# Optimization experiments

Measured on AMD Instinct MI355X. Metric: run time of the kernel, lower is better.

The kernel has to match this reference:

```python
import jax, jax.numpy as jnp
import numpy as np

N, D_IN, D, E, B = 30000, 512, 512, 300000, 4096
N_RES, N_DNN = 2, 2
EPS = 1e-5


def _ln(x, g, b):
    mu = jnp.mean(x, axis=-1, keepdims=True)
    var = jnp.mean((x - mu) ** 2, axis=-1, keepdims=True)
    return (x - mu) * jax.lax.rsqrt(var + EPS) * g + b


def setup_inputs() -> dict:
    key = jax.random.key(0)
    ks = jax.random.split(key, 16)
    s = 1.0 / np.sqrt(D)
    inp = {
        "node_feat": jax.random.normal(ks[0], (N, D_IN), jnp.float32),
        "edge_hop0": jax.random.randint(ks[1], (2, E), 0, N, jnp.int32),
        "edge_hop1": jax.random.randint(ks[2], (2, E), 0, N, jnp.int32),
        "target_idx": jax.random.randint(ks[3], (B,), 0, N, jnp.int32),
        # node transform
        "Wt": jax.random.normal(ks[4], (D_IN, D), jnp.float32) / np.sqrt(D_IN),
        "bt": jnp.zeros((D,), jnp.float32),
        # GATConv (shared across both hops, one relation)
        "Wf": jax.random.normal(ks[5], (D, D), jnp.float32) * s,
        "bf": jnp.zeros((D,), jnp.float32),
        "w_att": jax.random.normal(ks[6], (2 * D,), jnp.float32) * s,
        "b_att": jnp.zeros((), jnp.float32),
        "gat_bias": jnp.zeros((D,), jnp.float32),
        # Res_DNN
        "Wp": jax.random.normal(ks[7], (D, D), jnp.float32) * s,
        "bp": jnp.zeros((D,), jnp.float32),
        "dnn_W": jax.random.normal(ks[8], (N_RES, N_DNN, D, D), jnp.float32) * s,
        "dnn_b": jnp.zeros((N_RES, N_DNN, D), jnp.float32),
        "dnn_g": jnp.ones((N_RES, N_DNN, D), jnp.float32),
        "dnn_beta": jnp.zeros((N_RES, N_DNN, D), jnp.float32),
        "res_g": jnp.ones((N_RES, D), jnp.float32),
        "res_beta": jnp.zeros((N_RES, D), jnp.float32),
        "Wc": jax.random.normal(ks[9], (D, 1), jnp.float32) * s,
        "bc": jnp.zeros((1,), jnp.float32),
    }
    return inp


def _gat(feat, edges, Wf, bf, w_att, b_att, gat_bias):
    # dst and src are the same node set / same features here
    h = feat @ Wf + bf                      # [N, D]
    di, si = edges[0], edges[1]             # [E], [E]
    # att(concat(dst_h, src_h)) == dst_h @ w[:D] + src_h @ w[D:] + b
    sd = h @ w_att[:D]                      # [N]
    ss = h @ w_att[D:]                      # [N]
    e = jnp.tanh(sd[di] + ss[si] + b_att)   # [E]
    # sparse softmax per destination row
    m = jax.ops.segment_max(e, di, num_segments=N)
    a = jnp.exp(e - m[di])
    denom = jax.ops.segment_sum(a, di, num_segments=N)
    alpha = a / denom[di]                   # [E]
    # sparse-mm aggregation
    out = jax.ops.segment_sum(alpha[:, None] * h[si], di, num_segments=N)
    return out + gat_bias


def reference(node_feat, edge_hop0, edge_hop1, target_idx, Wt, bt, Wf, bf,
              w_att, b_att, gat_bias, Wp, bp, dnn_W, dnn_b, dnn_g, dnn_beta,
              res_g, res_beta, Wc, bc):
    # node-type feature transform (dropout is identity at inference)
    feat = node_feat @ Wt + bt              # [N, D]
    # hops processed from last to first: hop1 then hop0
    for edges in (edge_hop1, edge_hop0):
        g = _gat(feat, edges, Wf, bf, w_att, b_att, gat_bias)
        feat = (feat + g) * 0.5             # mean of stacked [orig, gat_out]
    h = feat[target_idx]                    # [B, D]
    # Res_DNN head
    h = h @ Wp + bp
    for r in range(N_RES):
        sc = h
        for i in range(N_DNN):
            h = _ln(jnp.tanh(h @ dnn_W[r, i] + dnn_b[r, i]), dnn_g[r, i], dnn_beta[r, i])
        h = _ln(jnp.tanh(sc + h), res_g[r], res_beta[r])
    logits = h @ Wc + bc                    # [B, 1]
    return jax.nn.sigmoid(logits)
```

## Files before the change

kernel.cpp:

```cpp
#include <hip/hip_runtime.h>

#define D 512
typedef unsigned short ushort_t;
typedef __attribute__((ext_vector_type(8))) short bf16x8;
typedef __attribute__((ext_vector_type(4))) float f32x4;

static __device__ __forceinline__ ushort_t f2bf(float f) {
  unsigned u = __float_as_uint(f);
  u += 0x7fffu + ((u >> 16) & 1u);
  return (ushort_t)(u >> 16);
}
static __device__ __forceinline__ float bf2f(ushort_t h) {
  return __uint_as_float(((unsigned)h) << 16);
}

static __device__ __forceinline__ void gld_lds16(const void* g, void* lds) {
  __builtin_amdgcn_global_load_lds(
      (const __attribute__((address_space(1))) unsigned int*)g,
      (__attribute__((address_space(3))) unsigned int*)lds, 16, 0, 0);
}

__global__ __launch_bounds__(256) void pack_weight(
    const float* __restrict__ W, ushort_t* __restrict__ out, int K, int N, int nmat) {
  int i = blockIdx.x * 256 + threadIdx.x;
  const int per = K * N;
  if (i >= per * nmat) return;
  const int mat = i / per;
  const int r = i - mat * per;
  const int k = r / N, n = r - k * N;
  const int nt = n >> 4, col = n & 15, kt = k >> 5, kg = (k >> 3) & 3, j = k & 7;
  out[(size_t)mat * per + (((size_t)nt * (K >> 5) + kt) << 9) + ((kg << 4) + col) * 8 + j] =
      f2bf(W[(size_t)mat * per + r]);
}

__global__ __launch_bounds__(256) void conv_bf16_pad(
    const float* __restrict__ in, ushort_t* __restrict__ out, int M, int Mp, int K) {
  const size_t i4 = ((size_t)blockIdx.x * 256 + threadIdx.x) * 4;
  if (i4 >= (size_t)Mp * K) return;
  const int row = (int)(i4 / K);
  ushort4 o;
  if (row < M) {
    const float4 v = *reinterpret_cast<const float4*>(&in[i4]);
    o.x = f2bf(v.x); o.y = f2bf(v.y); o.z = f2bf(v.z); o.w = f2bf(v.w);
  } else {
    o.x = o.y = o.z = o.w = 0;
  }
  *reinterpret_cast<ushort4*>(&out[i4]) = o;
}

__global__ __launch_bounds__(256) void gemm_mfma(
    const ushort_t* __restrict__ A, const ushort_t* __restrict__ Bp,
    const float* __restrict__ bias, ushort_t* __restrict__ C16, int N, int K) {
  __shared__ __align__(16) ushort_t As[2][8 * 512];
  __shared__ __align__(16) ushort_t Bs[2][8 * 512];
  const int nwg = gridDim.x;
  const int q = nwg >> 3, rm = nwg & 7;
  const int xcd = blockIdx.x & 7, kk = blockIdx.x >> 3;
  const int lin = (xcd < rm ? xcd * (q + 1) : rm * (q + 1) + (xcd - rm) * q) + kk;
  const int m0 = (lin >> 2) * 128;
  const int n0 = (lin & 3) * 128;
  const int tid = threadIdx.x;
  const int lane = tid & 63;
  const int wid = tid >> 6;
  const int wm = wid >> 1, wn = wid & 1;
  const int arow = lane & 15;
  const int akoff = (lane >> 4) * 8;
  const int kt32 = K >> 5;
  f32x4 acc[4][4] = {};

  auto stage = [&](int kt, int b) {
    const int k0 = kt * 32;
    gld_lds16(&A[(size_t)(m0 + (wid * 2 + 0) * 16 + arow) * K + k0 + akoff],
              &As[b][(wid * 2 + 0) * 512]);
    gld_lds16(&A[(size_t)(m0 + (wid * 2 + 1) * 16 + arow) * K + k0 + akoff],
              &As[b][(wid * 2 + 1) * 512]);
    gld_lds16(&Bp[(((size_t)(n0 / 16 + wid * 2 + 0) * kt32 + kt) << 9) + lane * 8],
              &Bs[b][(wid * 2 + 0) * 512]);
    gld_lds16(&Bp[(((size_t)(n0 / 16 + wid * 2 + 1) * kt32 + kt) << 9) + lane * 8],
              &Bs[b][(wid * 2 + 1) * 512]);
  };

  stage(0, 0);
  __syncthreads();
  int cur = 0;
  for (int t = 0; t < kt32; ++t) {
    if (t + 1 < kt32) stage(t + 1, cur ^ 1);
    bf16x8 af[4], bfr[4];
#pragma unroll
    for (int mi = 0; mi < 4; ++mi)
      af[mi] = *reinterpret_cast<const bf16x8*>(&As[cur][(wm * 4 + mi) * 512 + lane * 8]);
#pragma unroll
    for (int ni = 0; ni < 4; ++ni)
      bfr[ni] = *reinterpret_cast<const bf16x8*>(&Bs[cur][(wn * 4 + ni) * 512 + lane * 8]);
#pragma unroll
    for (int mi = 0; mi < 4; ++mi)
#pragma unroll
      for (int ni = 0; ni < 4; ++ni)
        acc[mi][ni] = __builtin_amdgcn_mfma_f32_16x16x32_bf16(af[mi], bfr[ni], acc[mi][ni], 0, 0, 0);
    __syncthreads();
    cur ^= 1;
  }
#pragma unroll
  for (int mi = 0; mi < 4; ++mi) {
    const int row = m0 + wm * 64 + mi * 16 + ((lane >> 4) << 2);
#pragma unroll
    for (int ni = 0; ni < 4; ++ni) {
      const int col = n0 + wn * 64 + ni * 16 + (lane & 15);
      const float bv = bias[col];
#pragma unroll
      for (int r = 0; r < 4; ++r)
        C16[(size_t)(row + r) * N + col] = f2bf(acc[mi][ni][r] + bv);
    }
  }
}

__global__ __launch_bounds__(256) void rowdot2_w(
    const ushort_t* __restrict__ hb, const float* __restrict__ w_att,
    float* __restrict__ sd, float* __restrict__ ss, int Nn) {
  const int r = blockIdx.x * 4 + (threadIdx.x >> 6);
  const int lane = threadIdx.x & 63;
  if (r >= Nn) return;
  const bf16x8 hv = *reinterpret_cast<const bf16x8*>(&hb[(size_t)r * D + lane * 8]);
  float d0 = 0.f, d1 = 0.f;
#pragma unroll
  for (int q = 0; q < 8; ++q) {
    const float v = bf2f((ushort_t)hv[q]);
    d0 += v * w_att[lane * 8 + q];
    d1 += v * w_att[D + lane * 8 + q];
  }
#pragma unroll
  for (int off = 32; off > 0; off >>= 1) {
    d0 += __shfl_xor(d0, off);
    d1 += __shfl_xor(d1, off);
  }
  if (lane == 0) { sd[r] = d0; ss[r] = d1; }
}

__global__ void fill_bucket(const int* __restrict__ e1, const int* __restrict__ e0,
                            int* __restrict__ cnt, int* __restrict__ bucket,
                            int Nn, int E) {
  const int e = blockIdx.x * blockDim.x + threadIdx.x;
  if (e >= E) return;
  const int d1 = e1[e];
  const int p1 = atomicAdd(&cnt[d1], 1);
  if (p1 < 64) bucket[(size_t)d1 * 64 + p1] = e1[E + e];
  const int d0 = e0[e];
  const int p0 = atomicAdd(&cnt[Nn + d0], 1);
  if (p0 < 64) bucket[((size_t)(Nn + d0)) * 64 + p0] = e0[E + e];
}

__global__ __launch_bounds__(256) void gat_aggregate_w(
    ushort_t* __restrict__ featb, const ushort_t* __restrict__ hb,
    const float* __restrict__ sd, const float* __restrict__ ss,
    const int* __restrict__ di, const int* __restrict__ si,
    const float* __restrict__ b_att_p, const float* __restrict__ gat_bias,
    const int* __restrict__ cnt, const int* __restrict__ bucket, int Nn, int E) {
  const int dst = blockIdx.x * 4 + (threadIdx.x >> 6);
  const int lane = threadIdx.x & 63;
  if (dst >= Nn) return;
  const int deg = cnt[dst];
  const float sdd = sd[dst];
  const float ba = b_att_p[0];
  const size_t o = (size_t)dst * D + lane * 8;
  bf16x8 fv = *reinterpret_cast<const bf16x8*>(&featb[o]);
  float acc[8] = {};
  if (deg <= 64) {
    const bool valid = lane < deg;
    const int slane = valid ? bucket[(size_t)dst * 64 + lane] : 0;
    const float e = valid ? tanhf(sdd + ss[slane] + ba) : -1e30f;
    float m = e;
#pragma unroll
    for (int off = 32; off > 0; off >>= 1) m = fmaxf(m, __shfl_xor(m, off));
    const float a = valid ? expf(e - m) : 0.f;
    float s = a;
#pragma unroll
    for (int off = 32; off > 0; off >>= 1) s += __shfl_xor(s, off);
    const float w = a * ((s > 0.f) ? 1.f / s : 0.f);
    int k = 0;
    for (; k + 7 < deg; k += 8) {
      float wk[8];
      int sk[8];
#pragma unroll
      for (int u = 0; u < 8; ++u) {
        wk[u] = __shfl(w, k + u);
        sk[u] = __shfl(slane, k + u);
      }
      bf16x8 hv[8];
#pragma unroll
      for (int u = 0; u < 8; ++u)
        hv[u] = *reinterpret_cast<const bf16x8*>(&hb[(size_t)sk[u] * D + lane * 8]);
#pragma unroll
      for (int qq = 0; qq < 8; ++qq) {
        float t0 = wk[0] * bf2f((ushort_t)hv[0][qq]) + wk[1] * bf2f((ushort_t)hv[1][qq]);
        float t1 = wk[2] * bf2f((ushort_t)hv[2][qq]) + wk[3] * bf2f((ushort_t)hv[3][qq]);
        float t2 = wk[4] * bf2f((ushort_t)hv[4][qq]) + wk[5] * bf2f((ushort_t)hv[5][qq]);
        float t3 = wk[6] * bf2f((ushort_t)hv[6][qq]) + wk[7] * bf2f((ushort_t)hv[7][qq]);
        acc[qq] += (t0 + t1) + (t2 + t3);
      }
    }
    for (; k + 1 < deg; k += 2) {
      const float w0 = __shfl(w, k), w1 = __shfl(w, k + 1);
      const int s0 = __shfl(slane, k), s1 = __shfl(slane, k + 1);
      const bf16x8 h0 = *reinterpret_cast<const bf16x8*>(&hb[(size_t)s0 * D + lane * 8]);
      const bf16x8 h1 = *reinterpret_cast<const bf16x8*>(&hb[(size_t)s1 * D + lane * 8]);
#pragma unroll
      for (int qq = 0; qq < 8; ++qq)
        acc[qq] += w0 * bf2f((ushort_t)h0[qq]) + w1 * bf2f((ushort_t)h1[qq]);
    }
    if (k < deg) {
      const float wk = __shfl(w, k);
      const int sk = __shfl(slane, k);
      const bf16x8 h0 = *reinterpret_cast<const bf16x8*>(&hb[(size_t)sk * D + lane * 8]);
#pragma unroll
      for (int qq = 0; qq < 8; ++qq) acc[qq] += wk * bf2f((ushort_t)h0[qq]);
    }
  } else {
    float m = -1e30f;
    for (int e = lane; e < E; e += 64)
      if (di[e] == dst) m = fmaxf(m, tanhf(sdd + ss[si[e]] + ba));
#pragma unroll
    for (int off = 32; off > 0; off >>= 1) m = fmaxf(m, __shfl_xor(m, off));
    float s = 0.f;
    for (int e = lane; e < E; e += 64)
      if (di[e] == dst) s += expf(tanhf(sdd + ss[si[e]] + ba) - m);
#pragma unroll
    for (int off = 32; off > 0; off >>= 1) s += __shfl_xor(s, off);
    const float inv = (s > 0.f) ? 1.f / s : 0.f;
    for (int base = 0; base < E; base += 64) {
      const int e = base + lane;
      const bool hit = (e < E) && (di[e] == dst);
      unsigned long long mask = __ballot(hit);
      const int sidx = hit ? si[e] : 0;
      const float aval = hit ? expf(tanhf(sdd + ss[sidx] + ba) - m) * inv : 0.f;
      while (mask) {
        const int l = __ffsll((long long)mask) - 1;
        mask &= mask - 1;
        const float wv = __shfl(aval, l);
        const int sk = __shfl(sidx, l);
        const bf16x8 hv = *reinterpret_cast<const bf16x8*>(&hb[(size_t)sk * D + lane * 8]);
#pragma unroll
        for (int qq = 0; qq < 8; ++qq) acc[qq] += wv * bf2f((ushort_t)hv[qq]);
      }
    }
  }
#pragma unroll
  for (int q = 0; q < 8; ++q) {
    const float f = (bf2f((ushort_t)fv[q]) + acc[q] + gat_bias[lane * 8 + q]) * 0.5f;
    fv[q] = (short)f2bf(f);
  }
  *reinterpret_cast<bf16x8*>(&featb[o]) = fv;
}

__global__ __launch_bounds__(1024, 4) void head_fused(
    const ushort_t* __restrict__ featb, const int* __restrict__ tidx,
    const ushort_t* __restrict__ pWp, const float* __restrict__ bp,
    const ushort_t* __restrict__ pDW, const float* __restrict__ dnn_b,
    const float* __restrict__ dnn_g, const float* __restrict__ dnn_be,
    const float* __restrict__ res_g, const float* __restrict__ res_be,
    const float* __restrict__ Wc, const float* __restrict__ bc,
    float* __restrict__ out) {
  __shared__ __align__(16) ushort_t A_lds[16 * 512];
  __shared__ float lsum[16][16], lsq[16][16], meanv[16], rsv[16];
  const int tid = threadIdx.x;
  const int lane = tid & 63;
  const int wave = tid >> 6;
  const int nt0 = wave * 2;
  const int c15 = lane & 15;
  const int rgrp = lane >> 4;

  {
    const int row = tid >> 6, col8 = tid & 63;
    const int g = tidx[blockIdx.x * 16 + row];
    const bf16x8 v = *reinterpret_cast<const bf16x8*>(&featb[(size_t)g * D + col8 * 8]);
    *reinterpret_cast<bf16x8*>(&A_lds[row * 512 + (col8 ^ (row & 7)) * 8]) = v;
  }
  __syncthreads();

  auto do_gemm = [&](const ushort_t* __restrict__ W, f32x4& a0, f32x4& a1) {
    a0 = f32x4{0.f, 0.f, 0.f, 0.f};
    a1 = f32x4{0.f, 0.f, 0.f, 0.f};
    bf16x8 c0 = *reinterpret_cast<const bf16x8*>(
        &W[(((size_t)nt0 * 16 + 0) << 9) + lane * 8]);
    bf16x8 c1 = *reinterpret_cast<const bf16x8*>(
        &W[(((size_t)(nt0 + 1) * 16 + 0) << 9) + lane * 8]);
#pragma unroll
    for (int kt = 0; kt < 16; ++kt) {
      bf16x8 n0 = c0, n1 = c1;
      if (kt < 15) {
        n0 = *reinterpret_cast<const bf16x8*>(
            &W[(((size_t)nt0 * 16 + kt + 1) << 9) + lane * 8]);
        n1 = *reinterpret_cast<const bf16x8*>(
            &W[(((size_t)(nt0 + 1) * 16 + kt + 1) << 9) + lane * 8]);
      }
      const int col8 = kt * 4 + rgrp;
      const bf16x8 af = *reinterpret_cast<const bf16x8*>(
          &A_lds[c15 * 512 + (col8 ^ (c15 & 7)) * 8]);
      a0 = __builtin_amdgcn_mfma_f32_16x16x32_bf16(af, c0, a0, 0, 0, 0);
      a1 = __builtin_amdgcn_mfma_f32_16x16x32_bf16(af, c1, a1, 0, 0, 0);
      c0 = n0;
      c1 = n1;
    }
  };

  auto block_ln = [&](f32x4& v0, f32x4& v1, const float* __restrict__ g,
                      const float* __restrict__ be) {
    float psum[4], psq[4];
#pragma unroll
    for (int r = 0; r < 4; ++r) {
      psum[r] = v0[r] + v1[r];
      psq[r] = v0[r] * v0[r] + v1[r] * v1[r];
    }
#pragma unroll
    for (int off = 8; off > 0; off >>= 1)
#pragma unroll
      for (int r = 0; r < 4; ++r) {
        psum[r] += __shfl_xor(psum[r], off);
        psq[r] += __shfl_xor(psq[r], off);
      }
    if (c15 == 0) {
#pragma unroll
      for (int r = 0; r < 4; ++r) {
        lsum[wave][rgrp * 4 + r] = psum[r];
        lsq[wave][rgrp * 4 + r] = psq[r];
      }
    }
    __syncthreads();
    if (tid < 16) {
      float s = 0.f, qq = 0.f;
#pragma unroll
      for (int w = 0; w < 16; ++w) { s += lsum[w][tid]; qq += lsq[w][tid]; }
      const float mean = s * (1.f / 512.f);
      const float var = qq * (1.f / 512.f) - mean * mean;
      meanv[tid] = mean;
      rsv[tid] = rsqrtf(var + 1e-5f);
    }
    __syncthreads();
    const int col0 = nt0 * 16 + c15;
    const int col1 = (nt0 + 1) * 16 + c15;
    const float g0 = g[col0], b0 = be[col0];
    const float g1 = g[col1], b1 = be[col1];
#pragma unroll
    for (int r = 0; r < 4; ++r) {
      const int row = rgrp * 4 + r;
      v0[r] = (v0[r] - meanv[row]) * rsv[row] * g0 + b0;
      v1[r] = (v1[r] - meanv[row]) * rsv[row] * g1 + b1;
    }
  };

  auto store_A = [&](const f32x4& v0, const f32x4& v1) {
    const int col0 = nt0 * 16 + c15;
    const int col1 = (nt0 + 1) * 16 + c15;
#pragma unroll
    for (int r = 0; r < 4; ++r) {
      const int row = rgrp * 4 + r;
      A_lds[row * 512 + (((col0 >> 3) ^ (row & 7)) << 3) + (col0 & 7)] = f2bf(v0[r]);
      A_lds[row * 512 + (((col1 >> 3) ^ (row & 7)) << 3) + (col1 & 7)] = f2bf(v1[r]);
    }
  };

  f32x4 sc0, sc1, acc0, acc1, ln0, ln1;

  do_gemm(pWp, acc0, acc1);
  {
    const float bv0 = bp[nt0 * 16 + c15];
    const float bv1 = bp[(nt0 + 1) * 16 + c15];
#pragma unroll
    for (int r = 0; r < 4; ++r) { sc0[r] = acc0[r] + bv0; sc1[r] = acc1[r] + bv1; }
  }
  __syncthreads();
  store_A(sc0, sc1);
  __syncthreads();

  for (int rb = 0; rb < 2; ++rb) {
    {
      const int st = rb * 2;
      do_gemm(pDW + (size_t)st * D * D, acc0, acc1);
      const float bv0 = dnn_b[st * D + nt0 * 16 + c15];
      const float bv1 = dnn_b[st * D + (nt0 + 1) * 16 + c15];
#pragma unroll
      for (int r = 0; r < 4; ++r) {
        acc0[r] = tanhf(acc0[r] + bv0);
        acc1[r] = tanhf(acc1[r] + bv1);
      }
      block_ln(acc0, acc1, dnn_g + st * D, dnn_be + st * D);
      store_A(acc0, acc1);
      __syncthreads();
    }
    {
      const int st = rb * 2 + 1;
      do_gemm(pDW + (size_t)st * D * D, ln0, ln1);
      const float bv0 = dnn_b[st * D + nt0 * 16 + c15];
      const float bv1 = dnn_b[st * D + (nt0 + 1) * 16 + c15];
#pragma unroll
      for (int r = 0; r < 4; ++r) {
        ln0[r] = tanhf(ln0[r] + bv0);
        ln1[r] = tanhf(ln1[r] + bv1);
      }
      block_ln(ln0, ln1, dnn_g + st * D, dnn_be + st * D);
    }
#pragma unroll
    for (int r = 0; r < 4; ++r) {
      acc0[r] = tanhf(sc0[r] + ln0[r]);
      acc1[r] = tanhf(sc1[r] + ln1[r]);
    }
    block_ln(acc0, acc1, res_g + rb * D, res_be + rb * D);
    sc0 = acc0;
    sc1 = acc1;
    if (rb == 0) {
      store_A(sc0, sc1);
      __syncthreads();
    }
  }

  float pr[4];
  {
    const float w0 = Wc[nt0 * 16 + c15];
    const float w1 = Wc[(nt0 + 1) * 16 + c15];
#pragma unroll
    for (int r = 0; r < 4; ++r) pr[r] = sc0[r] * w0 + sc1[r] * w1;
  }
#pragma unroll
  for (int off = 8; off > 0; off >>= 1)
#pragma unroll
    for (int r = 0; r < 4; ++r) pr[r] += __shfl_xor(pr[r], off);
  __syncthreads();
  if (c15 == 0) {
#pragma unroll
    for (int r = 0; r < 4; ++r) lsum[wave][rgrp * 4 + r] = pr[r];
  }
  __syncthreads();
  if (tid < 16) {
    float s = 0.f;
#pragma unroll
    for (int w = 0; w < 16; ++w) s += lsum[w][tid];
    out[blockIdx.x * 16 + tid] = 1.f / (1.f + expf(-(s + bc[0])));
  }
}

extern "C" void kernel_launch(void* const* d_in, const int* in_sizes, int n_in,
                              void* d_out, int out_size, void* d_ws, size_t ws_size,
                              hipStream_t stream) {
  (void)n_in; (void)out_size; (void)ws_size;
  const float* node_feat = (const float*)d_in[0];
  const int* edge0 = (const int*)d_in[1];
  const int* edge1 = (const int*)d_in[2];
  const int* tidx = (const int*)d_in[3];
  const float* Wt = (const float*)d_in[4];
  const float* bt = (const float*)d_in[5];
  const float* Wf = (const float*)d_in[6];
  const float* bfp = (const float*)d_in[7];
  const float* w_att = (const float*)d_in[8];
  const float* b_att = (const float*)d_in[9];
  const float* gat_bias = (const float*)d_in[10];
  const float* Wp = (const float*)d_in[11];
  const float* bp = (const float*)d_in[12];
  const float* dnn_W = (const float*)d_in[13];
  const float* dnn_b = (const float*)d_in[14];
  const float* dnn_g = (const float*)d_in[15];
  const float* dnn_be = (const float*)d_in[16];
  const float* res_g = (const float*)d_in[17];
  const float* res_be = (const float*)d_in[18];
  const float* Wc = (const float*)d_in[19];
  const float* bc = (const float*)d_in[20];
  float* out = (float*)d_out;

  const int Nn = in_sizes[0] / D;
  const int E = in_sizes[1] / 2;
  const int B = in_sizes[3];
  const int K_IN = in_sizes[4] / D;
  const int Mp = (Nn + 127) / 128 * 128;
  const int N2 = 2 * Nn;

  char* p = (char*)d_ws;
  auto alloc = [&](size_t bytes) -> char* {
    char* r = p;
    p += (bytes + 255) & ~(size_t)255;
    return r;
  };
  ushort_t* featb = (ushort_t*)alloc((size_t)Mp * D * 2);
  ushort_t* hb = (ushort_t*)alloc((size_t)Mp * D * 2);
  float* sd = (float*)alloc((size_t)Nn * 4);
  float* ss = (float*)alloc((size_t)Nn * 4);
  int* cnt = (int*)alloc((size_t)N2 * 4);
  int* bucket = (int*)alloc((size_t)N2 * 64 * 4);
  ushort_t* pWt = (ushort_t*)alloc((size_t)K_IN * D * 2);
  ushort_t* pWf = (ushort_t*)alloc((size_t)D * D * 2);
  ushort_t* pWp = (ushort_t*)alloc((size_t)D * D * 2);
  ushort_t* pDWall = (ushort_t*)alloc((size_t)4 * D * D * 2);

  dim3 blk(256);
  const int nw4 = (Nn + 3) / 4;

  {
    pack_weight<<<(K_IN * D + 255) / 256, blk, 0, stream>>>(Wt, pWt, K_IN, D, 1);
    pack_weight<<<(D * D + 255) / 256, blk, 0, stream>>>(Wf, pWf, D, D, 1);
    pack_weight<<<(D * D + 255) / 256, blk, 0, stream>>>(Wp, pWp, D, D, 1);
    pack_weight<<<(4 * D * D + 255) / 256, blk, 0, stream>>>(dnn_W, pDWall, D, D, 4);
    conv_bf16_pad<<<((size_t)Mp * K_IN / 4 + 255) / 256, blk, 0, stream>>>(
        node_feat, hb , Nn, Mp, K_IN);
  }

  hipMemsetAsync(cnt, 0, (size_t)N2 * 4, stream);
  fill_bucket<<<(E + 255) / 256, blk, 0, stream>>>(edge1, edge0, cnt, bucket, Nn, E);

  gemm_mfma<<<dim3(4 * (Mp / 128)), blk, 0, stream>>>(hb, pWt, bt, featb, D, K_IN);

  const int* hops[2] = {edge1, edge0};
  for (int hp = 0; hp < 2; ++hp) {
    gemm_mfma<<<dim3(4 * (Mp / 128)), blk, 0, stream>>>(featb, pWf, bfp, hb, D, D);
    rowdot2_w<<<nw4, blk, 0, stream>>>(hb, w_att, sd, ss, Nn);
    gat_aggregate_w<<<nw4, blk, 0, stream>>>(
        featb, hb, sd, ss, hops[hp], hops[hp] + E, b_att, gat_bias,
        cnt + hp * Nn, bucket + (size_t)hp * Nn * 64, Nn, E);
  }

  head_fused<<<B / 16, dim3(1024), 0, stream>>>(
      featb, tidx, pWp, bp, pDWall, dnn_b, dnn_g, dnn_be, res_g, res_be,
      Wc, bc, out);
}
```

Baseline: 340.7 us.

## Split GEMM tile across 8 waves and aggregation rows across two waves

The MFMA GEMM now launches 512 threads per block, so eight waves each compute a 32x64 sub-tile of the 128x128 output instead of four waves each computing 64x64. Each wave now stages one A and one B 16-row slice, which halves the accumulator registers per wave. The GAT aggregation assigns two waves per destination node, each handling 256 columns with 4-element bf16 loads and a 4-wide unrolled neighbour loop instead of 8-wide. The goal is more waves in flight to hide gather and MFMA latency, at the cost of narrower 8-byte loads and recomputing the per-row softmax in both waves.

Result: no change. 340.2 us (-0.1%).

```diff
diff --git a/kernel.cpp b/kernel.cpp
--- a/kernel.cpp
+++ b/kernel.cpp
@@ -3,6 +3,7 @@
 #define D 512
 typedef unsigned short ushort_t;
 typedef __attribute__((ext_vector_type(8))) short bf16x8;
+typedef __attribute__((ext_vector_type(4))) short bf16x4;
 typedef __attribute__((ext_vector_type(4))) float f32x4;
 
 static __device__ __forceinline__ ushort_t f2bf(float f) {
@@ -48,7 +49,7 @@
   *reinterpret_cast<ushort4*>(&out[i4]) = o;
 }
 
-__global__ __launch_bounds__(256) void gemm_mfma(
+__global__ __launch_bounds__(512) void gemm_mfma(
     const ushort_t* __restrict__ A, const ushort_t* __restrict__ Bp,
     const float* __restrict__ bias, ushort_t* __restrict__ C16, int N, int K) {
   __shared__ __align__(16) ushort_t As[2][8 * 512];
@@ -62,22 +63,19 @@
   const int tid = threadIdx.x;
   const int lane = tid & 63;
   const int wid = tid >> 6;
-  const int wm = wid >> 1, wn = wid & 1;
+  const int wm = wid >> 1;
+  const int wn = wid & 1;
   const int arow = lane & 15;
   const int akoff = (lane >> 4) * 8;
   const int kt32 = K >> 5;
-  f32x4 acc[4][4] = {};
+  f32x4 acc[2][4] = {};
 
   auto stage = [&](int kt, int b) {
     const int k0 = kt * 32;
-    gld_lds16(&A[(size_t)(m0 + (wid * 2 + 0) * 16 + arow) * K + k0 + akoff],
-              &As[b][(wid * 2 + 0) * 512]);
-    gld_lds16(&A[(size_t)(m0 + (wid * 2 + 1) * 16 + arow) * K + k0 + akoff],
-              &As[b][(wid * 2 + 1) * 512]);
-    gld_lds16(&Bp[(((size_t)(n0 / 16 + wid * 2 + 0) * kt32 + kt) << 9) + lane * 8],
-              &Bs[b][(wid * 2 + 0) * 512]);
-    gld_lds16(&Bp[(((size_t)(n0 / 16 + wid * 2 + 1) * kt32 + kt) << 9) + lane * 8],
-              &Bs[b][(wid * 2 + 1) * 512]);
+    gld_lds16(&A[(size_t)(m0 + wid * 16 + arow) * K + k0 + akoff],
+              &As[b][wid * 512]);
+    gld_lds16(&Bp[(((size_t)(n0 / 16 + wid) * kt32 + kt) << 9) + lane * 8],
+              &Bs[b][wid * 512]);
   };
 
   stage(0, 0);
@@ -85,15 +83,15 @@
   int cur = 0;
   for (int t = 0; t < kt32; ++t) {
     if (t + 1 < kt32) stage(t + 1, cur ^ 1);
-    bf16x8 af[4], bfr[4];
-#pragma unroll
-    for (int mi = 0; mi < 4; ++mi)
-      af[mi] = *reinterpret_cast<const bf16x8*>(&As[cur][(wm * 4 + mi) * 512 + lane * 8]);
+    bf16x8 af[2], bfr[4];
+#pragma unroll
+    for (int mi = 0; mi < 2; ++mi)
+      af[mi] = *reinterpret_cast<const bf16x8*>(&As[cur][(wm * 2 + mi) * 512 + lane * 8]);
 #pragma unroll
     for (int ni = 0; ni < 4; ++ni)
       bfr[ni] = *reinterpret_cast<const bf16x8*>(&Bs[cur][(wn * 4 + ni) * 512 + lane * 8]);
 #pragma unroll
-    for (int mi = 0; mi < 4; ++mi)
+    for (int mi = 0; mi < 2; ++mi)
 #pragma unroll
       for (int ni = 0; ni < 4; ++ni)
         acc[mi][ni] = __builtin_amdgcn_mfma_f32_16x16x32_bf16(af[mi], bfr[ni], acc[mi][ni], 0, 0, 0);
@@ -101,8 +99,8 @@
     cur ^= 1;
   }
 #pragma unroll
-  for (int mi = 0; mi < 4; ++mi) {
-    const int row = m0 + wm * 64 + mi * 16 + ((lane >> 4) << 2);
+  for (int mi = 0; mi < 2; ++mi) {
+    const int row = m0 + wm * 32 + mi * 16 + ((lane >> 4) << 2);
 #pragma unroll
     for (int ni = 0; ni < 4; ++ni) {
       const int col = n0 + wn * 64 + ni * 16 + (lane & 15);
@@ -155,15 +153,17 @@
     const int* __restrict__ di, const int* __restrict__ si,
     const float* __restrict__ b_att_p, const float* __restrict__ gat_bias,
     const int* __restrict__ cnt, const int* __restrict__ bucket, int Nn, int E) {
-  const int dst = blockIdx.x * 4 + (threadIdx.x >> 6);
+  const int wave = threadIdx.x >> 6;
+  const int dst = blockIdx.x * 2 + (wave >> 1);
   const int lane = threadIdx.x & 63;
   if (dst >= Nn) return;
+  const int colb = (wave & 1) * 256 + lane * 4;
   const int deg = cnt[dst];
   const float sdd = sd[dst];
   const float ba = b_att_p[0];
-  const size_t o = (size_t)dst * D + lane * 8;
-  bf16x8 fv = *reinterpret_cast<const bf16x8*>(&featb[o]);
-  float acc[8] = {};
+  const size_t o = (size_t)dst * D + colb;
+  bf16x4 fv = *reinterpret_cast<const bf16x4*>(&featb[o]);
+  float acc[4] = {};
   if (deg <= 64) {
     const bool valid = lane < deg;
     const int slane = valid ? bucket[(size_t)dst * 64 + lane] : 0;
@@ -177,42 +177,28 @@
     for (int off = 32; off > 0; off >>= 1) s += __shfl_xor(s, off);
     const float w = a * ((s > 0.f) ? 1.f / s : 0.f);
     int k = 0;
-    for (; k + 7 < deg; k += 8) {
-      float wk[8];
-      int sk[8];
-#pragma unroll
-      for (int u = 0; u < 8; ++u) {
-        wk[u] = __shfl(w, k + u);
-        sk[u] = __shfl(slane, k + u);
-      }
-      bf16x8 hv[8];
-#pragma unroll
-      for (int u = 0; u < 8; ++u)
-        hv[u] = *reinterpret_cast<const bf16x8*>(&hb[(size_t)sk[u] * D + lane * 8]);
-#pragma unroll
-      for (int qq = 0; qq < 8; ++qq) {
-        float t0 = wk[0] * bf2f((ushort_t)hv[0][qq]) + wk[1] * bf2f((ushort_t)hv[1][qq]);
-        float t1 = wk[2] * bf2f((ushort_t)hv[2][qq]) + wk[3] * bf2f((ushort_t)hv[3][qq]);
-        float t2 = wk[4] * bf2f((ushort_t)hv[4][qq]) + wk[5] * bf2f((ushort_t)hv[5][qq]);
-        float t3 = wk[6] * bf2f((ushort_t)hv[6][qq]) + wk[7] * bf2f((ushort_t)hv[7][qq]);
-        acc[qq] += (t0 + t1) + (t2 + t3);
-      }
-    }
-    for (; k + 1 < deg; k += 2) {
+    for (; k + 3 < deg; k += 4) {
       const float w0 = __shfl(w, k), w1 = __shfl(w, k + 1);
+      const float w2 = __shfl(w, k + 2), w3 = __shfl(w, k + 3);
       const int s0 = __shfl(slane, k), s1 = __shfl(slane, k + 1);
-      const bf16x8 h0 = *reinterpret_cast<const bf16x8*>(&hb[(size_t)s0 * D + lane * 8]);
-      const bf16x8 h1 = *reinterpret_cast<const bf16x8*>(&hb[(size_t)s1 * D + lane * 8]);
-#pragma unroll
-      for (int qq = 0; qq < 8; ++qq)
-        acc[qq] += w0 * bf2f((ushort_t)h0[qq]) + w1 * bf2f((ushort_t)h1[qq]);
-    }
-    if (k < deg) {
+      const int s2 = __shfl(slane, k + 2), s3 = __shfl(slane, k + 3);
+      const bf16x4 h0 = *reinterpret_cast<const bf16x4*>(&hb[(size_t)s0 * D + colb]);
+      const bf16x4 h1 = *reinterpret_cast<const bf16x4*>(&hb[(size_t)s1 * D + colb]);
+      const bf16x4 h2 = *reinterpret_cast<const bf16x4*>(&hb[(size_t)s2 * D + colb]);
+      const bf16x4 h3 = *reinterpret_cast<const bf16x4*>(&hb[(size_t)s3 * D + colb]);
+#pragma unroll
+      for (int qq = 0; qq < 4; ++qq) {
+        const float t0 = w0 * bf2f((ushort_t)h0[qq]) + w1 * bf2f((ushort_t)h1[qq]);
+        const float t1 = w2 * bf2f((ushort_t)h2[qq]) + w3 * bf2f((ushort_t)h3[qq]);
+        acc[qq] += t0 + t1;
+      }
+    }
+    for (; k < deg; ++k) {
       const float wk = __shfl(w, k);
       const int sk = __shfl(slane, k);
-      const bf16x8 h0 = *reinterpret_cast<const bf16x8*>(&hb[(size_t)sk * D + lane * 8]);
-#pragma unroll
-      for (int qq = 0; qq < 8; ++qq) acc[qq] += wk * bf2f((ushort_t)h0[qq]);
+      const bf16x4 h0 = *reinterpret_cast<const bf16x4*>(&hb[(size_t)sk * D + colb]);
+#pragma unroll
+      for (int qq = 0; qq < 4; ++qq) acc[qq] += wk * bf2f((ushort_t)h0[qq]);
     }
   } else {
     float m = -1e30f;
@@ -237,18 +223,18 @@
         mask &= mask - 1;
         const float wv = __shfl(aval, l);
         const int sk = __shfl(sidx, l);
-        const bf16x8 hv = *reinterpret_cast<const bf16x8*>(&hb[(size_t)sk * D + lane * 8]);
-#pragma unroll
-        for (int qq = 0; qq < 8; ++qq) acc[qq] += wv * bf2f((ushort_t)hv[qq]);
-      }
-    }
-  }
-#pragma unroll
-  for (int q = 0; q < 8; ++q) {
-    const float f = (bf2f((ushort_t)fv[q]) + acc[q] + gat_bias[lane * 8 + q]) * 0.5f;
+        const bf16x4 hv = *reinterpret_cast<const bf16x4*>(&hb[(size_t)sk * D + colb]);
+#pragma unroll
+        for (int qq = 0; qq < 4; ++qq) acc[qq] += wv * bf2f((ushort_t)hv[qq]);
+      }
+    }
+  }
+#pragma unroll
+  for (int q = 0; q < 4; ++q) {
+    const float f = (bf2f((ushort_t)fv[q]) + acc[q] + gat_bias[colb + q]) * 0.5f;
     fv[q] = (short)f2bf(f);
   }
-  *reinterpret_cast<bf16x8*>(&featb[o]) = fv;
+  *reinterpret_cast<bf16x4*>(&featb[o]) = fv;
 }
 
 __global__ __launch_bounds__(1024, 4) void head_fused(
@@ -489,7 +475,7 @@
   ushort_t* pDWall = (ushort_t*)alloc((size_t)4 * D * D * 2);
 
   dim3 blk(256);
-  const int nw4 = (Nn + 3) / 4;
+  const int nw2 = (Nn + 1) / 2;
 
   {
     pack_weight<<<(K_IN * D + 255) / 256, blk, 0, stream>>>(Wt, pWt, K_IN, D, 1);
@@ -503,13 +489,13 @@
   hipMemsetAsync(cnt, 0, (size_t)N2 * 4, stream);
   fill_bucket<<<(E + 255) / 256, blk, 0, stream>>>(edge1, edge0, cnt, bucket, Nn, E);
 
-  gemm_mfma<<<dim3(4 * (Mp / 128)), blk, 0, stream>>>(hb, pWt, bt, featb, D, K_IN);
+  gemm_mfma<<<dim3(4 * (Mp / 128)), dim3(512), 0, stream>>>(hb, pWt, bt, featb, D, K_IN);
 
   const int* hops[2] = {edge1, edge0};
   for (int hp = 0; hp < 2; ++hp) {
-    gemm_mfma<<<dim3(4 * (Mp / 128)), blk, 0, stream>>>(featb, pWf, bfp, hb, D, D);
-    rowdot2_w<<<nw4, blk, 0, stream>>>(hb, w_att, sd, ss, Nn);
-    gat_aggregate_w<<<nw4, blk, 0, stream>>>(
+    gemm_mfma<<<dim3(4 * (Mp / 128)), dim3(512), 0, stream>>>(featb, pWf, bfp, hb, D, D);
+    rowdot2_w<<<(Nn + 3) / 4, blk, 0, stream>>>(hb, w_att, sd, ss, Nn);
+    gat_aggregate_w<<<nw2, blk, 0, stream>>>(
         featb, hb, sd, ss, hops[hp], hops[hp] + E, b_att, gat_bias,
         cnt + hp * Nn, bucket + (size_t)hp * Nn * 64, Nn, E);
   }
```
